# Kernel tuning notes

Measured on AMD Instinct MI355X. Metric: run time of the kernel, lower is better.

## Reference

```python
import jax, jax.numpy as jnp
import numpy as np
from jax import lax

N, L, V, ES, HS = 16384, 512, 32000, 32, 64


def setup_inputs() -> dict:
    key = jax.random.key(0)
    k_tok, k_len, k_emb, k_wih, k_whh, k_bih, k_bhh = jax.random.split(key, 7)
    # valid tokens in [1, V) so that (x != 0).sum(1) == true prefix length
    tok = jax.random.randint(k_tok, (N, L), 1, V)
    lengths = jax.random.randint(k_len, (N,), 0, L + 1)  # includes empty seqs
    x = jnp.where(jnp.arange(L)[None, :] < lengths[:, None], tok, 0)
    s = 0.1
    embedding = jax.random.normal(k_emb, (V, ES), dtype=jnp.float32) * s
    w_ih = jax.random.normal(k_wih, (3 * HS, ES), dtype=jnp.float32) * s  # [r|z|n] stacked (torch order)
    w_hh = jax.random.normal(k_whh, (3 * HS, HS), dtype=jnp.float32) * s
    b_ih = jax.random.normal(k_bih, (3 * HS,), dtype=jnp.float32) * s
    b_hh = jax.random.normal(k_bhh, (3 * HS,), dtype=jnp.float32) * s
    return {"x": x, "embedding": embedding, "w_ih": w_ih, "w_hh": w_hh,
            "b_ih": b_ih, "b_hh": b_hh}


def reference(x, embedding, w_ih, w_hh, b_ih, b_hh):
    # Faithful math: final GRU hidden state over the nonzero prefix of each row;
    # rows with length 0 return zeros (h0). Equivalent to bucketed
    # pack_padded_sequence + GRU + scatter of final hidden states.
    n, l = x.shape
    hs = w_hh.shape[1]
    lengths = (x != 0).sum(axis=1)  # [n]

    def step(h, inp):
        t, xt = inp                      # xt: [n] token ids at time t
        e = embedding[xt]                # [n, es] gather
        gx = e @ w_ih.T + b_ih           # [n, 3*hs]
        gh = h @ w_hh.T + b_hh           # [n, 3*hs]
        xr, xz, xn = jnp.split(gx, 3, axis=-1)
        hr, hz, hn = jnp.split(gh, 3, axis=-1)
        r = jax.nn.sigmoid(xr + hr)
        z = jax.nn.sigmoid(xz + hz)
        ng = jnp.tanh(xn + r * hn)
        h_new = (1.0 - z) * ng + z * h   # torch GRU update
        h = jnp.where((t < lengths)[:, None], h_new, h)  # freeze past length
        return h, None

    h0 = jnp.zeros((n, hs), dtype=embedding.dtype)
    hT, _ = lax.scan(step, h0, (jnp.arange(l), x.T))
    return hT
```

## Files before the change

### kernel.cpp

```cpp
#include <hip/hip_runtime.h>

#define N_SEQ 16384
#define LSEQ  512
#define VOCAB 32000
#define ES    32
#define HS    64
#define LDH   72
#define TS    18
#define RT    1024
#define NCH   (N_SEQ / 2)
#define NBLK  (NCH / 16)

#define SC_RZ (-1.4426950408889634f)
#define SC_N  (-2.8853900817779268f)

typedef _Float16 v8h __attribute__((ext_vector_type(8)));
typedef float    v4f __attribute__((ext_vector_type(4)));

__global__ __launch_bounds__(256) void k_len(const int* __restrict__ x,
                                             int* __restrict__ len,
                                             int* __restrict__ hist){
  int row = blockIdx.x * 256 + threadIdx.x;
  const int* xr = x + (size_t)row * LSEQ;
  int lo = 0, hi = LSEQ;
  while (lo < hi){ int mid = (lo + hi) >> 1; if (xr[mid] != 0) lo = mid + 1; else hi = mid; }
  len[row] = lo;
  atomicAdd(&hist[lo], 1);
}

#define SCB   16
#define EMBV  125
__global__ __launch_bounds__(1024) void k_mid(const int* __restrict__ hist,
                                              const int* __restrict__ len,
                                              int* __restrict__ gcnt,
                                              int* __restrict__ perm,
                                              const float* __restrict__ emb,
                                              const float* __restrict__ whh,
                                              const float* __restrict__ wih,
                                              _Float16* __restrict__ ef,
                                              _Float16* __restrict__ wpk,
                                              _Float16* __restrict__ wpe){
  int b = blockIdx.x;
  if (b < SCB){
    __shared__ int buf[1024];
    __shared__ int offs[513];
    int i = threadIdx.x;
    buf[i] = (i < 513) ? hist[i] : 0;
    __syncthreads();
    for (int d = 1; d < 1024; d <<= 1){
      int v = (i >= d) ? buf[i - d] : 0;
      __syncthreads();
      buf[i] += v;
      __syncthreads();
    }
    if (i < 513) offs[i] = (i == 0) ? 0 : buf[i - 1];
    __syncthreads();
    int s = b * 1024 + i;
    int l = len[s];
    int pos = offs[l] + atomicAdd(&gcnt[l], 1);
    perm[pos] = s;
  } else if (b < SCB + EMBV){
    int i = ((b - SCB) * 1024 + threadIdx.x) * 8;
    float4 f0 = *(const float4*)(emb + i);
    float4 f1 = *(const float4*)(emb + i + 4);
    v8h o;
    o[0] = (_Float16)f0.x; o[1] = (_Float16)f0.y;
    o[2] = (_Float16)f0.z; o[3] = (_Float16)f0.w;
    o[4] = (_Float16)f1.x; o[5] = (_Float16)f1.y;
    o[6] = (_Float16)f1.z; o[7] = (_Float16)f1.w;
    *(v8h*)(ef + i) = o;
  } else {
    int tid = (b - SCB - EMBV) * 1024 + threadIdx.x;
    if (tid < 1536){
      int f = tid >> 6, l = tid & 63;
      int jt = f >> 1, kf = f & 1;
      float sc = (jt < 8) ? SC_RZ : SC_N;
      #pragma unroll
      for (int i = 0; i < 8; ++i){
        int row = jt * 16 + (l & 15);
        int col = kf * 32 + (l >> 4) * 8 + i;
        wpk[(size_t)tid * 8 + i] = (_Float16)(sc * whh[row * HS + col]);
      }
    } else if (tid < 1536 + 768){
      int t2 = tid - 1536;
      int tile = t2 >> 6, l = t2 & 63;
      float sc = ((tile >> 2) < 2) ? SC_RZ : SC_N;
      #pragma unroll
      for (int i = 0; i < 8; ++i){
        int row = tile * 16 + (l & 15);
        int col = (l >> 4) * 8 + i;
        wpe[(size_t)t2 * 8 + i] = (_Float16)(sc * wih[row * ES + col]);
      }
    }
  }
}

__global__ __launch_bounds__(256, 2) void k_gru(
    const int* __restrict__ x, const _Float16* __restrict__ ef,
    const _Float16* __restrict__ wpk, const _Float16* __restrict__ wpe,
    const float* __restrict__ bih, const float* __restrict__ bhh,
    const int* __restrict__ perm, const int* __restrict__ len,
    float* __restrict__ out)
{
  __shared__ __align__(16) _Float16 hb[2][16 * LDH];
  __shared__ unsigned short tok[RT * TS];
  __shared__ int sA[16], sB[16], sLA[16], sLB[16];
  int qt   = threadIdx.x >> 6;
  int grp  = blockIdx.x;
  int lane = threadIdx.x & 63;
  int q = lane >> 4, c = lane & 15;
  int uu = qt*16 + c;

  v8h bfh[3][2], bfe[3];
  #pragma unroll
  for (int g = 0; g < 3; ++g){
    int tile = g*4 + qt;
    #pragma unroll
    for (int kf = 0; kf < 2; ++kf)
      bfh[g][kf] = *(const v8h*)(wpk + ((size_t)(tile*2 + kf)*64 + lane)*8);
    bfe[g] = *(const v8h*)(wpe + ((size_t)tile*64 + lane)*8);
  }

  if (threadIdx.x < 16){
    int ch = grp*16 + threadIdx.x;
    int a  = perm[(N_SEQ - 1) - ch];
    int b2 = perm[ch];
    sA[threadIdx.x] = a;  sB[threadIdx.x] = b2;
    sLA[threadIdx.x] = len[a]; sLB[threadIdx.x] = len[b2];
  }
  for (int i = threadIdx.x; i < 16*LDH; i += 256) hb[0][i] = (_Float16)0.f;
  __syncthreads();

  int sqA[4], sqB[4], lnA[4], lnT[4];
  #pragma unroll
  for (int r = 0; r < 4; ++r){
    int s0 = q*4 + r;
    sqA[r] = sA[s0];  sqB[r] = sB[s0];
    lnA[r] = sLA[s0]; lnT[r] = sLA[s0] + sLB[s0];
  }

  float br  = SC_RZ * (bih[uu]      + bhh[uu]);
  float bz  = SC_RZ * (bih[HS + uu] + bhh[HS + uu]);
  float ben = SC_N  *  bih[2*HS + uu];
  float bhn = SC_N  *  bhh[2*HS + uu];
  v4f brq  = {br, br, br, br};
  v4f bzq  = {bz, bz, bz, bz};
  v4f benq = {ben, ben, ben, ben};
  v4f bhnq = {bhn, bhn, bhn, bhn};

  float h[4];
  #pragma unroll
  for (int r = 0; r < 4; ++r) h[r] = 0.f;

  for (int j = threadIdx.x; j < 16*RT; j += 256){
    int s = j >> 10, tt = j & (RT-1);
    int la  = sLA[s];
    int isA = tt < la;
    int tb  = tt - la; tb = tb < 511 ? tb : 511;
    int seq = isA ? sA[s] : sB[s];
    int tc  = isA ? tt : tb;
    tok[tt*TS + s] = (unsigned short)x[(size_t)seq * LSEQ + tc];
  }
  __syncthreads();

  int tmax = max(max(lnT[0], lnT[1]), max(lnT[2], lnT[3]));
  tmax = max(tmax, __shfl_xor(tmax, 16, 64));
  tmax = max(tmax, __shfl_xor(tmax, 32, 64));
  int tmin = min(min(lnT[0], lnT[1]), min(lnT[2], lnT[3]));
  tmin = min(tmin, __shfl_xor(tmin, 16, 64));
  tmin = min(tmin, __shfl_xor(tmin, 32, 64));

  v8h aec, aen;
  v4f pra, prb, pza, pzb, dea, deb;
  {
    int tk0 = tok[0*TS + c];
    aec = *(const v8h*)(ef + (size_t)tk0 * ES + q*8);
    pra = __builtin_amdgcn_mfma_f32_16x16x32_f16(aec, bfe[0], brq,  0,0,0);
    pza = __builtin_amdgcn_mfma_f32_16x16x32_f16(aec, bfe[1], bzq,  0,0,0);
    dea = __builtin_amdgcn_mfma_f32_16x16x32_f16(aec, bfe[2], benq, 0,0,0);
    int tk1 = tok[1*TS + c];
    aen = *(const v8h*)(ef + (size_t)tk1 * ES + q*8);
  }

  #define GRU_STEP(FREEZE, ACONS, ALOAD, PRR, PRZ, DEN, PRRn, PRZn, DENn, RB, WB) \
  {                                                                            \
    int tkn = tok[((t + 2) & (RT-1))*TS + c];                                  \
    v8h a0 = *(const v8h*)(&hb[RB][c*LDH + q*8]);                              \
    v8h a1 = *(const v8h*)(&hb[RB][c*LDH + 32 + q*8]);                         \
    v4f zr  = __builtin_amdgcn_mfma_f32_16x16x32_f16(a1, bfh[0][1], PRR, 0,0,0);\
    v4f Dr  = __builtin_amdgcn_mfma_f32_16x16x32_f16(a0, bfh[0][0], zr,  0,0,0);\
    v4f zz  = __builtin_amdgcn_mfma_f32_16x16x32_f16(a1, bfh[1][1], PRZ, 0,0,0);\
    v4f Dz  = __builtin_amdgcn_mfma_f32_16x16x32_f16(a0, bfh[1][0], zz,  0,0,0);\
    v4f zh  = __builtin_amdgcn_mfma_f32_16x16x32_f16(a1, bfh[2][1], bhnq,0,0,0);\
    v4f Dhn = __builtin_amdgcn_mfma_f32_16x16x32_f16(a0, bfh[2][0], zh,  0,0,0);\
    _Pragma("unroll")                                                          \
    for (int r = 0; r < 4; ++r){                                               \
      float rg   = __builtin_amdgcn_rcpf(1.f + __builtin_amdgcn_exp2f(Dr[r])); \
      float zg   = __builtin_amdgcn_rcpf(1.f + __builtin_amdgcn_exp2f(Dz[r])); \
      float te   = __builtin_amdgcn_exp2f(DEN[r] + rg * Dhn[r]);               \
      float ng   = fmaf(2.f, __builtin_amdgcn_rcpf(1.f + te), -1.f);           \
      float hnew = ng + zg * (h[r] - ng);                                      \
      h[r]       = (FREEZE && t >= lnT[r]) ? h[r] : hnew;                      \
    }                                                                          \
    {                                                                          \
      int f0 = (t + 1 == lnA[0]), f1 = (t + 1 == lnA[1]);                      \
      int f2 = (t + 1 == lnA[2]), f3 = (t + 1 == lnA[3]);                      \
      if (f0 | f1 | f2 | f3){                                                  \
        if (f0){ out[(size_t)sqA[0]*HS + uu] = h[0]; h[0] = 0.f; }             \
        if (f1){ out[(size_t)sqA[1]*HS + uu] = h[1]; h[1] = 0.f; }             \
        if (f2){ out[(size_t)sqA[2]*HS + uu] = h[2]; h[2] = 0.f; }             \
        if (f3){ out[(size_t)sqA[3]*HS + uu] = h[3]; h[3] = 0.f; }             \
      }                                                                        \
    }                                                                          \
    PRRn = __builtin_amdgcn_mfma_f32_16x16x32_f16(ACONS, bfe[0], brq,  0,0,0); \
    PRZn = __builtin_amdgcn_mfma_f32_16x16x32_f16(ACONS, bfe[1], bzq,  0,0,0); \
    DENn = __builtin_amdgcn_mfma_f32_16x16x32_f16(ACONS, bfe[2], benq, 0,0,0); \
    ALOAD = *(const v8h*)(ef + (size_t)tkn * ES + q*8);           \
    _Pragma("unroll")                                                          \
    for (int r = 0; r < 4; ++r)                                                \
      hb[WB][(q*4 + r)*LDH + uu] = (_Float16)h[r];                             \
    asm volatile("s_waitcnt lgkmcnt(0)" ::: "memory");                         \
    __builtin_amdgcn_s_barrier();                                              \
    asm volatile("" ::: "memory");                                             \
  }

  int t = 0;
  for (; t + 1 < tmin; ){
    GRU_STEP(0, aen, aec, pra, pza, dea, prb, pzb, deb, 0, 1); ++t;
    GRU_STEP(0, aec, aen, prb, pzb, deb, pra, pza, dea, 1, 0); ++t;
  }
  for (; t + 1 < tmax; ){
    GRU_STEP(1, aen, aec, pra, pza, dea, prb, pzb, deb, 0, 1); ++t;
    GRU_STEP(1, aec, aen, prb, pzb, deb, pra, pza, dea, 1, 0); ++t;
  }
  if (t < tmax){
    GRU_STEP(1, aen, aec, pra, pza, dea, prb, pzb, deb, 0, 1); ++t;
  }
  #undef GRU_STEP

  #pragma unroll
  for (int r = 0; r < 4; ++r){
    out[(size_t)sqB[r]*HS + uu] = h[r];
    if (lnA[r] == 0) out[(size_t)sqA[r]*HS + uu] = 0.f;
  }
}

extern "C" void kernel_launch(void* const* d_in, const int* in_sizes, int n_in,
                              void* d_out, int out_size, void* d_ws, size_t ws_size,
                              hipStream_t stream){
  const int*   x   = (const int*)  d_in[0];
  const float* emb = (const float*)d_in[1];
  const float* wih = (const float*)d_in[2];
  const float* whh = (const float*)d_in[3];
  const float* bih = (const float*)d_in[4];
  const float* bhh = (const float*)d_in[5];
  float* out = (float*)d_out;

  char* ws = (char*)d_ws;
  size_t off = 0;
  _Float16* ef  = (_Float16*)(ws + off);  off += (size_t)VOCAB * ES * sizeof(_Float16);
  _Float16* wpk = (_Float16*)(ws + off);  off += (size_t)24 * 64 * 8 * sizeof(_Float16);
  _Float16* wpe = (_Float16*)(ws + off);  off += (size_t)12 * 64 * 8 * sizeof(_Float16);
  off = (off + 255) & ~(size_t)255;
  int* len  = (int*)(ws + off);           off += (size_t)N_SEQ * sizeof(int);
  int* perm = (int*)(ws + off);           off += (size_t)N_SEQ * sizeof(int);
  int* hist = (int*)(ws + off);           off += 513 * sizeof(int);
  int* gcnt = (int*)(ws + off);           off += 513 * sizeof(int);

  hipMemsetAsync(hist, 0, 2 * 513 * sizeof(int), stream);
  k_len <<<N_SEQ / 256, 256, 0, stream>>>(x, len, hist);
  k_mid <<<SCB + EMBV + 3, 1024, 0, stream>>>(hist, len, gcnt, perm,
                                              emb, whh, wih, ef, wpk, wpe);
  k_gru <<<NBLK, 256, 0, stream>>>(x, ef, wpk, wpe, bih, bhh, perm, len, out);
}
```

Measured before the change: 354.5 us.

## Interleave two independent GRU chain groups per block and vectorize length counting

Each GRU block now processes two independent 16-chain groups, interleaving their recurrent steps so one group's MFMA and transcendental latency can overlap with the other's. Each round uses a single barrier for both groups, and there are 256 blocks at one block per CU instead of two smaller blocks per CU. The length kernel switches from a per-thread binary search to a wavefront-wide vectorized nonzero count with a shuffle reduction, giving coalesced reads. The cost is higher register pressure and a combined step count set by the slowest of 32 chains per block.

```diff
diff --git a/kernel.cpp b/kernel.cpp
--- a/kernel.cpp
+++ b/kernel.cpp
@@ -8,8 +8,7 @@
 #define LDH   72
 #define TS    18
 #define RT    1024
-#define NCH   (N_SEQ / 2)
-#define NBLK  (NCH / 16)
+#define NBLK  256
 
 #define SC_RZ (-1.4426950408889634f)
 #define SC_N  (-2.8853900817779268f)
@@ -20,12 +19,18 @@
 __global__ __launch_bounds__(256) void k_len(const int* __restrict__ x,
                                              int* __restrict__ len,
                                              int* __restrict__ hist){
-  int row = blockIdx.x * 256 + threadIdx.x;
-  const int* xr = x + (size_t)row * LSEQ;
-  int lo = 0, hi = LSEQ;
-  while (lo < hi){ int mid = (lo + hi) >> 1; if (xr[mid] != 0) lo = mid + 1; else hi = mid; }
-  len[row] = lo;
-  atomicAdd(&hist[lo], 1);
+  int row  = blockIdx.x * 4 + (threadIdx.x >> 6);
+  int lane = threadIdx.x & 63;
+  const int4* xr = (const int4*)(x + (size_t)row * LSEQ);
+  int cnt = 0;
+  #pragma unroll
+  for (int i = 0; i < 2; ++i){
+    int4 v = xr[lane + i*64];
+    cnt += (v.x != 0) + (v.y != 0) + (v.z != 0) + (v.w != 0);
+  }
+  #pragma unroll
+  for (int d = 1; d < 64; d <<= 1) cnt += __shfl_xor(cnt, d, 64);
+  if (lane == 0){ len[row] = cnt; atomicAdd(&hist[cnt], 1); }
 }
 
 #define SCB   16
@@ -95,18 +100,19 @@
   }
 }
 
-__global__ __launch_bounds__(256, 2) void k_gru(
+__global__ __launch_bounds__(256, 1) void k_gru(
     const int* __restrict__ x, const _Float16* __restrict__ ef,
     const _Float16* __restrict__ wpk, const _Float16* __restrict__ wpe,
     const float* __restrict__ bih, const float* __restrict__ bhh,
     const int* __restrict__ perm, const int* __restrict__ len,
     float* __restrict__ out)
 {
-  __shared__ __align__(16) _Float16 hb[2][16 * LDH];
-  __shared__ unsigned short tok[RT * TS];
-  __shared__ int sA[16], sB[16], sLA[16], sLB[16];
+  __shared__ __align__(16) _Float16 hbA[2][16 * LDH];
+  __shared__ __align__(16) _Float16 hbB[2][16 * LDH];
+  __shared__ unsigned short tokA[(RT + 2) * TS];
+  __shared__ unsigned short tokB[(RT + 2) * TS];
+  __shared__ int sP[32], sQ[32], sL1[32], sL2[32];
   int qt   = threadIdx.x >> 6;
-  int grp  = blockIdx.x;
   int lane = threadIdx.x & 63;
   int q = lane >> 4, c = lane & 15;
   int uu = qt*16 + c;
@@ -121,22 +127,28 @@
     bfe[g] = *(const v8h*)(wpe + ((size_t)tile*64 + lane)*8);
   }
 
-  if (threadIdx.x < 16){
-    int ch = grp*16 + threadIdx.x;
-    int a  = perm[(N_SEQ - 1) - ch];
-    int b2 = perm[ch];
-    sA[threadIdx.x] = a;  sB[threadIdx.x] = b2;
-    sLA[threadIdx.x] = len[a]; sLB[threadIdx.x] = len[b2];
-  }
-  for (int i = threadIdx.x; i < 16*LDH; i += 256) hb[0][i] = (_Float16)0.f;
+  if (threadIdx.x < 32){
+    int ch = blockIdx.x*32 + threadIdx.x;
+    int p  = perm[(N_SEQ - 1) - ch];
+    int q2 = perm[ch];
+    sP[threadIdx.x] = p;       sQ[threadIdx.x] = q2;
+    sL1[threadIdx.x] = len[p]; sL2[threadIdx.x] = len[q2];
+  }
+  for (int i = threadIdx.x; i < 16*LDH; i += 256){
+    hbA[0][i] = (_Float16)0.f;
+    hbB[0][i] = (_Float16)0.f;
+  }
   __syncthreads();
 
-  int sqA[4], sqB[4], lnA[4], lnT[4];
+  int psA[4], qsA[4], lnPA[4], lnTA[4];
+  int psB[4], qsB[4], lnPB[4], lnTB[4];
   #pragma unroll
   for (int r = 0; r < 4; ++r){
-    int s0 = q*4 + r;
-    sqA[r] = sA[s0];  sqB[r] = sB[s0];
-    lnA[r] = sLA[s0]; lnT[r] = sLA[s0] + sLB[s0];
+    int j = q*4 + r;
+    psA[r] = sP[j];      qsA[r] = sQ[j];
+    lnPA[r] = sL1[j];    lnTA[r] = sL1[j] + sL2[j];
+    psB[r] = sP[j+16];   qsB[r] = sQ[j+16];
+    lnPB[r] = sL1[j+16]; lnTB[r] = sL1[j+16] + sL2[j+16];
   }
 
   float br  = SC_RZ * (bih[uu]      + bhh[uu]);
@@ -148,45 +160,62 @@
   v4f benq = {ben, ben, ben, ben};
   v4f bhnq = {bhn, bhn, bhn, bhn};
 
-  float h[4];
-  #pragma unroll
-  for (int r = 0; r < 4; ++r) h[r] = 0.f;
-
-  for (int j = threadIdx.x; j < 16*RT; j += 256){
-    int s = j >> 10, tt = j & (RT-1);
-    int la  = sLA[s];
-    int isA = tt < la;
-    int tb  = tt - la; tb = tb < 511 ? tb : 511;
-    int seq = isA ? sA[s] : sB[s];
+  float hA[4], hB[4];
+  #pragma unroll
+  for (int r = 0; r < 4; ++r){ hA[r] = 0.f; hB[r] = 0.f; }
+
+  for (int i = threadIdx.x; i < 32*RT; i += 256){
+    int ch = i >> 10, tt = i & (RT-1);
+    int l1 = sL1[ch];
+    int isA = tt < l1;
+    int tb = tt - l1; tb = tb < 511 ? tb : 511;
+    int seq = isA ? sP[ch] : sQ[ch];
     int tc  = isA ? tt : tb;
-    tok[tt*TS + s] = (unsigned short)x[(size_t)seq * LSEQ + tc];
+    unsigned short v = (unsigned short)x[(size_t)seq * LSEQ + tc];
+    if (ch < 16) tokA[tt*TS + ch] = v; else tokB[tt*TS + (ch-16)] = v;
+  }
+  if (threadIdx.x < 64){
+    int g = threadIdx.x >> 5, rr = (threadIdx.x >> 4) & 1, s = threadIdx.x & 15;
+    (g ? tokB : tokA)[(RT + rr)*TS + s] = 0;
   }
   __syncthreads();
 
-  int tmax = max(max(lnT[0], lnT[1]), max(lnT[2], lnT[3]));
+  int tmax = 0, tmin = RT;
+  #pragma unroll
+  for (int r = 0; r < 4; ++r){
+    tmax = max(tmax, max(lnTA[r], lnTB[r]));
+    tmin = min(tmin, min(lnTA[r], lnTB[r]));
+  }
   tmax = max(tmax, __shfl_xor(tmax, 16, 64));
   tmax = max(tmax, __shfl_xor(tmax, 32, 64));
-  int tmin = min(min(lnT[0], lnT[1]), min(lnT[2], lnT[3]));
   tmin = min(tmin, __shfl_xor(tmin, 16, 64));
   tmin = min(tmin, __shfl_xor(tmin, 32, 64));
 
-  v8h aec, aen;
-  v4f pra, prb, pza, pzb, dea, deb;
+  v8h aecA, aenA, aecB, aenB;
+  v4f praA, prbA, pzaA, pzbA, deaA, debA;
+  v4f praB, prbB, pzaB, pzbB, deaB, debB;
   {
-    int tk0 = tok[0*TS + c];
-    aec = *(const v8h*)(ef + (size_t)tk0 * ES + q*8);
-    pra = __builtin_amdgcn_mfma_f32_16x16x32_f16(aec, bfe[0], brq,  0,0,0);
-    pza = __builtin_amdgcn_mfma_f32_16x16x32_f16(aec, bfe[1], bzq,  0,0,0);
-    dea = __builtin_amdgcn_mfma_f32_16x16x32_f16(aec, bfe[2], benq, 0,0,0);
-    int tk1 = tok[1*TS + c];
-    aen = *(const v8h*)(ef + (size_t)tk1 * ES + q*8);
-  }
-
-  #define GRU_STEP(FREEZE, ACONS, ALOAD, PRR, PRZ, DEN, PRRn, PRZn, DENn, RB, WB) \
+    int tk0 = tokA[0*TS + c];
+    aecA = *(const v8h*)(ef + (size_t)tk0 * ES + q*8);
+    praA = __builtin_amdgcn_mfma_f32_16x16x32_f16(aecA, bfe[0], brq,  0,0,0);
+    pzaA = __builtin_amdgcn_mfma_f32_16x16x32_f16(aecA, bfe[1], bzq,  0,0,0);
+    deaA = __builtin_amdgcn_mfma_f32_16x16x32_f16(aecA, bfe[2], benq, 0,0,0);
+    int tk1 = tokA[1*TS + c];
+    aenA = *(const v8h*)(ef + (size_t)tk1 * ES + q*8);
+    int tk0b = tokB[0*TS + c];
+    aecB = *(const v8h*)(ef + (size_t)tk0b * ES + q*8);
+    praB = __builtin_amdgcn_mfma_f32_16x16x32_f16(aecB, bfe[0], brq,  0,0,0);
+    pzaB = __builtin_amdgcn_mfma_f32_16x16x32_f16(aecB, bfe[1], bzq,  0,0,0);
+    deaB = __builtin_amdgcn_mfma_f32_16x16x32_f16(aecB, bfe[2], benq, 0,0,0);
+    int tk1b = tokB[1*TS + c];
+    aenB = *(const v8h*)(ef + (size_t)tk1b * ES + q*8);
+  }
+
+  #define GRU_PHASE(TOK, HB, H, LNP, LNT, SEQP, PRR, PRZ, DEN, PRRn, PRZn, DENn, ACONS, ALOAD, FREEZE, RB, WB) \
   {                                                                            \
-    int tkn = tok[((t + 2) & (RT-1))*TS + c];                                  \
-    v8h a0 = *(const v8h*)(&hb[RB][c*LDH + q*8]);                              \
-    v8h a1 = *(const v8h*)(&hb[RB][c*LDH + 32 + q*8]);                         \
+    int tkn = TOK[(t + 2)*TS + c];                                             \
+    v8h a0 = *(const v8h*)(&HB[RB][c*LDH + q*8]);                              \
+    v8h a1 = *(const v8h*)(&HB[RB][c*LDH + 32 + q*8]);                         \
     v4f zr  = __builtin_amdgcn_mfma_f32_16x16x32_f16(a1, bfh[0][1], PRR, 0,0,0);\
     v4f Dr  = __builtin_amdgcn_mfma_f32_16x16x32_f16(a0, bfh[0][0], zr,  0,0,0);\
     v4f zz  = __builtin_amdgcn_mfma_f32_16x16x32_f16(a1, bfh[1][1], PRZ, 0,0,0);\
@@ -199,17 +228,17 @@
       float zg   = __builtin_amdgcn_rcpf(1.f + __builtin_amdgcn_exp2f(Dz[r])); \
       float te   = __builtin_amdgcn_exp2f(DEN[r] + rg * Dhn[r]);               \
       float ng   = fmaf(2.f, __builtin_amdgcn_rcpf(1.f + te), -1.f);           \
-      float hnew = ng + zg * (h[r] - ng);                                      \
-      h[r]       = (FREEZE && t >= lnT[r]) ? h[r] : hnew;                      \
+      float hnew = ng + zg * (H[r] - ng);                                      \
+      H[r]       = (FREEZE && t >= LNT[r]) ? H[r] : hnew;                      \
     }                                                                          \
     {                                                                          \
-      int f0 = (t + 1 == lnA[0]), f1 = (t + 1 == lnA[1]);                      \
-      int f2 = (t + 1 == lnA[2]), f3 = (t + 1 == lnA[3]);                      \
+      int f0 = (t + 1 == LNP[0]), f1 = (t + 1 == LNP[1]);                      \
+      int f2 = (t + 1 == LNP[2]), f3 = (t + 1 == LNP[3]);                      \
       if (f0 | f1 | f2 | f3){                                                  \
-        if (f0){ out[(size_t)sqA[0]*HS + uu] = h[0]; h[0] = 0.f; }             \
-        if (f1){ out[(size_t)sqA[1]*HS + uu] = h[1]; h[1] = 0.f; }             \
-        if (f2){ out[(size_t)sqA[2]*HS + uu] = h[2]; h[2] = 0.f; }             \
-        if (f3){ out[(size_t)sqA[3]*HS + uu] = h[3]; h[3] = 0.f; }             \
+        if (f0){ out[(size_t)SEQP[0]*HS + uu] = H[0]; H[0] = 0.f; }            \
+        if (f1){ out[(size_t)SEQP[1]*HS + uu] = H[1]; H[1] = 0.f; }            \
+        if (f2){ out[(size_t)SEQP[2]*HS + uu] = H[2]; H[2] = 0.f; }            \
+        if (f3){ out[(size_t)SEQP[3]*HS + uu] = H[3]; H[3] = 0.f; }            \
       }                                                                        \
     }                                                                          \
     PRRn = __builtin_amdgcn_mfma_f32_16x16x32_f16(ACONS, bfe[0], brq,  0,0,0); \
@@ -218,30 +247,45 @@
     ALOAD = *(const v8h*)(ef + (size_t)tkn * ES + q*8);           \
     _Pragma("unroll")                                                          \
     for (int r = 0; r < 4; ++r)                                                \
-      hb[WB][(q*4 + r)*LDH + uu] = (_Float16)h[r];                             \
+      HB[WB][(q*4 + r)*LDH + uu] = (_Float16)H[r];                             \
+  }
+
+  #define ROUND_EVEN(FREEZE)                                                   \
+    GRU_PHASE(tokA, hbA, hA, lnPA, lnTA, psA, praA,pzaA,deaA, prbA,pzbA,debA, aenA, aecA, FREEZE, 0, 1); \
+    GRU_PHASE(tokB, hbB, hB, lnPB, lnTB, psB, praB,pzaB,deaB, prbB,pzbB,debB, aenB, aecB, FREEZE, 0, 1); \
     asm volatile("s_waitcnt lgkmcnt(0)" ::: "memory");                         \
     __builtin_amdgcn_s_barrier();                                              \
-    asm volatile("" ::: "memory");                                             \
-  }
+    asm volatile("" ::: "memory");
+
+  #define ROUND_ODD(FREEZE)                                                    \
+    GRU_PHASE(tokA, hbA, hA, lnPA, lnTA, psA, prbA,pzbA,debA, praA,pzaA,deaA, aecA, aenA, FREEZE, 1, 0); \
+    GRU_PHASE(tokB, hbB, hB, lnPB, lnTB, psB, prbB,pzbB,debB, praB,pzaB,deaB, aecB, aenB, FREEZE, 1, 0); \
+    asm volatile("s_waitcnt lgkmcnt(0)" ::: "memory");                         \
+    __builtin_amdgcn_s_barrier();                                              \
+    asm volatile("" ::: "memory");
 
   int t = 0;
   for (; t + 1 < tmin; ){
-    GRU_STEP(0, aen, aec, pra, pza, dea, prb, pzb, deb, 0, 1); ++t;
-    GRU_STEP(0, aec, aen, prb, pzb, deb, pra, pza, dea, 1, 0); ++t;
+    ROUND_EVEN(0); ++t;
+    ROUND_ODD(0);  ++t;
   }
   for (; t + 1 < tmax; ){
-    GRU_STEP(1, aen, aec, pra, pza, dea, prb, pzb, deb, 0, 1); ++t;
-    GRU_STEP(1, aec, aen, prb, pzb, deb, pra, pza, dea, 1, 0); ++t;
+    ROUND_EVEN(1); ++t;
+    ROUND_ODD(1);  ++t;
   }
   if (t < tmax){
-    GRU_STEP(1, aen, aec, pra, pza, dea, prb, pzb, deb, 0, 1); ++t;
-  }
-  #undef GRU_STEP
+    ROUND_EVEN(1); ++t;
+  }
+  #undef ROUND_EVEN
+  #undef ROUND_ODD
+  #undef GRU_PHASE
 
   #pragma unroll
   for (int r = 0; r < 4; ++r){
-    out[(size_t)sqB[r]*HS + uu] = h[r];
-    if (lnA[r] == 0) out[(size_t)sqA[r]*HS + uu] = 0.f;
+    out[(size_t)qsA[r]*HS + uu] = hA[r];
+    out[(size_t)qsB[r]*HS + uu] = hB[r];
+    if (lnPA[r] == 0) out[(size_t)psA[r]*HS + uu] = 0.f;
+    if (lnPB[r] == 0) out[(size_t)psB[r]*HS + uu] = 0.f;
   }
 }
 
@@ -268,7 +312,7 @@
   int* gcnt = (int*)(ws + off);           off += 513 * sizeof(int);
 
   hipMemsetAsync(hist, 0, 2 * 513 * sizeof(int), stream);
-  k_len <<<N_SEQ / 256, 256, 0, stream>>>(x, len, hist);
+  k_len <<<N_SEQ / 4, 256, 0, stream>>>(x, len, hist);
   k_mid <<<SCB + EMBV + 3, 1024, 0, stream>>>(hist, len, gcnt, perm,
                                               emb, whh, wih, ef, wpk, wpe);
   k_gru <<<NBLK, 256, 0, stream>>>(x, ef, wpk, wpe, bih, bhh, perm, len, out);
```

Measured after the change: 489.1 us. 1.38x slower.
